# Optimization experiments

Measured on AMD Instinct MI355X. Metric: run time of the kernel, lower is better.

Reference implementation:

```python
import jax, jax.numpy as jnp
import numpy as np

B, T, E, NH = 2, 2048, 512, 8
HD = E // NH
SCALE = float(HD) ** -0.5


def setup_inputs() -> dict:
    key = jax.random.key(0)
    ks = jax.random.split(key, 7)
    s = 0.02
    return {
        "x": jax.random.normal(ks[0], (B, T, E), dtype=jnp.float32),
        "w_qkv": jax.random.normal(ks[1], (E, 3 * E), dtype=jnp.float32) * s,
        "b_qkv": jax.random.normal(ks[2], (3 * E,), dtype=jnp.float32) * s,
        "w_od": jax.random.normal(ks[3], (E, 2 * NH), dtype=jnp.float32) * s,
        "b_od": jax.random.normal(ks[4], (2 * NH,), dtype=jnp.float32) * s,
        "w_out": jax.random.normal(ks[5], (E, E), dtype=jnp.float32) * s,
        "b_out": jax.random.normal(ks[6], (E,), dtype=jnp.float32) * s,
    }


def _heads(t):  # (B,T,E) -> (B*NH, T, HD)
    return t.reshape(B, T, NH, HD).transpose(0, 2, 1, 3).reshape(B * NH, T, HD)


def _point_mask(idx, j):  # idx: (B*NH,T) float indices -> one-hot (B*NH,T,T)
    return (j[None, None, :] == idx[:, :, None]).astype(jnp.float32)


def reference(x, w_qkv, b_qkv, w_od, b_od, w_out, b_out):
    qkv = x @ w_qkv + b_qkv
    Q, K, V = jnp.split(qkv, 3, axis=-1)  # each (B,T,E)

    od = Q @ w_od + b_od  # (B,T,2*NH)
    offset, duration = jnp.split(od, 2, axis=-1)
    offset = jnp.tanh(offset) * T
    duration = jax.nn.sigmoid(duration) * T

    query_index = jnp.arange(T, dtype=x.dtype)[None, :, None]  # (1,T,1)
    anchor = query_index + offset  # (B,T,NH)
    # 'b t nh -> (b nh) t'
    anchor = anchor.transpose(0, 2, 1).reshape(B * NH, T)
    duration = duration.transpose(0, 2, 1).reshape(B * NH, T)

    start = anchor - duration
    end = anchor + duration
    bound_l = jnp.floor(start)
    bound_r = jnp.ceil(end)
    anchor_l = jnp.floor(anchor)
    anchor_r = anchor_l + 1.0

    j = jnp.arange(T, dtype=x.dtype)
    neg_bound_weight = (bound_l - start)[:, :, None] * _point_mask(bound_l, j) \
                     + (end - bound_r)[:, :, None] * _point_mask(bound_r, j)
    anchor_dist_l = anchor - anchor_l
    anchor_weight = anchor_dist_l[:, :, None] * _point_mask(anchor_r, j) \
                  + (1.0 - anchor_dist_l)[:, :, None] * _point_mask(anchor_l, j)
    point_weight = 1.0 + neg_bound_weight + anchor_weight  # (B*NH,T,T)

    # segment mask: True OUTSIDE [bound_l, bound_r]
    attn_mask = (j[None, None, :] < bound_l[:, :, None]) | (j[None, None, :] > bound_r[:, :, None])

    Qh, Kh, Vh = _heads(Q), _heads(K), _heads(V)  # (B*NH, T, HD)
    scores = jnp.einsum('bic,brc->bir', Qh, Kh) * SCALE * point_weight
    scores = jnp.where(attn_mask, jnp.asarray(-1e8, scores.dtype), scores)
    attn = jax.nn.softmax(scores, axis=-1)
    out = jnp.einsum('bir,brc->bic', attn, Vh)  # (B*NH,T,HD)
    out = out.reshape(B, NH, T, HD).transpose(0, 2, 1, 3).reshape(B, T, E)
    return out @ w_out + b_out
```

## Files before the change

### kernel.cpp

```cpp
#include <hip/hip_runtime.h>
#include <math.h>

typedef float vf4 __attribute__((ext_vector_type(4)));
typedef float f32x4 __attribute__((ext_vector_type(4)));
typedef short bf16x8 __attribute__((ext_vector_type(8)));
typedef short short4v __attribute__((ext_vector_type(4)));
typedef int int2v __attribute__((ext_vector_type(2)));
typedef int int4v __attribute__((ext_vector_type(4)));

constexpr int B = 2, T = 2048, E = 512, NH = 8, HD = 64;
constexpr int BH = B * NH;
constexpr int NT = BH * T;
constexpr int KSPLIT = 4;
constexpr float SCALE = 0.125f;
constexpr float LOG2E = 1.44269504088896f;
constexpr float QSC = SCALE * LOG2E;

static __device__ __forceinline__ short f2bf(float f) {
  unsigned u = __float_as_uint(f);
  unsigned r = (u + 0x7fffu + ((u >> 16) & 1u)) >> 16;
  return (short)r;
}
static __device__ __forceinline__ unsigned pk2bf(float a, float b) {
  unsigned lo = (unsigned)(unsigned short)f2bf(a);
  unsigned hi = (unsigned)(unsigned short)f2bf(b);
  return lo | (hi << 16);
}
static __device__ __forceinline__ unsigned pkhu(float a, float b) {
  unsigned ua = __float_as_uint(a) + 0x8000u;
  unsigned ub = __float_as_uint(b) + 0x8000u;
  return __builtin_amdgcn_perm(ub, ua, 0x07060302u);
}
#if __has_builtin(__builtin_amdgcn_exp2f)
#define EXP2F(x) __builtin_amdgcn_exp2f(x)
#else
#define EXP2F(x) exp2f(x)
#endif
static __device__ __forceinline__ float bf2f(short s) {
  return __uint_as_float(((unsigned)(unsigned short)s) << 16);
}

__global__ __launch_bounds__(256) void prep_all(
    const float* __restrict__ x, const float* __restrict__ w_qkv,
    const float* __restrict__ b_qkv, const float* __restrict__ w_od,
    const float* __restrict__ b_od,
    short* __restrict__ xb, short* __restrict__ wTq, short* __restrict__ wTo,
    const float* __restrict__ w_out, float* __restrict__ Wc,
    float* __restrict__ bc)
{
  __shared__ float sh[8464];
  const int bid = blockIdx.x;
  const int tid = threadIdx.x;

  if (bid < 2048) {
    int idx = (bid * 256 + tid) * 4;
    vf4 v = *(const vf4*)&x[idx];
    short4v o;
    o[0] = f2bf(v[0]); o[1] = f2bf(v[1]); o[2] = f2bf(v[2]); o[3] = f2bf(v[3]);
    *(short4v*)&xb[idx] = o;
  } else if (bid < 3072) {
    const float* w; short* wT; int N, t;
    if (bid < 2816) { t = bid - 2048; w = w_qkv; wT = wTq; N = 1536; }
    else            { t = bid - 2816; w = w_out; wT = wTo; N = 512; }
    float (*tt)[33] = (float(*)[33])sh;
    const int k0 = (t & 15) * 32;
    const int n0 = (t >> 4) * 32;
    const int c = tid & 31, r = tid >> 5;
#pragma unroll
    for (int p = 0; p < 4; ++p)
      tt[r + p * 8][c] = w[(size_t)(k0 + r + p * 8) * N + n0 + c];
    __syncthreads();
#pragma unroll
    for (int p = 0; p < 4; ++p)
      wT[(size_t)(n0 + r + p * 8) * 512 + k0 + c] = f2bf(tt[c][r + p * 8]);
  } else {
    float* Lod = sh;
    float (*pb)[17] = (float(*)[17])(sh + 8192);
    const int bx = bid - 3072;
#pragma unroll
    for (int p = 0; p < 8; ++p) {
      int idx = (p * 256 + tid) * 4;
      *(vf4*)&Lod[idx] = *(const vf4*)&w_od[idx];
    }
    __syncthreads();
    if (bx < 32) {
      const int k = bx * 16 + (tid >> 4);
      const int c = tid & 15;
      float s = 0.0f;
      for (int m = 0; m < E; m += 4) {
        vf4 wq = *(const vf4*)&w_qkv[(size_t)k * 1536 + m];
        s += wq[0] * Lod[(m + 0) * 16 + c] + wq[1] * Lod[(m + 1) * 16 + c]
           + wq[2] * Lod[(m + 2) * 16 + c] + wq[3] * Lod[(m + 3) * 16 + c];
      }
      Wc[k * 16 + c] = s;
    } else {
      const int c = tid & 15, seg = tid >> 4;
      float s = 0.0f;
      for (int m = seg * 32; m < seg * 32 + 32; ++m)
        s += b_qkv[m] * Lod[m * 16 + c];
      pb[seg][c] = s;
      __syncthreads();
      if (tid < 16) {
        float acc = b_od[tid];
#pragma unroll
        for (int g = 0; g < 16; ++g) acc += pb[g][tid];
        bc[tid] = acc;
      }
    }
  }
}

__global__ __launch_bounds__(256) void qkv_od(
    const short* __restrict__ xb, const short* __restrict__ wT,
    const float* __restrict__ bias, short* __restrict__ qkvb,
    short* __restrict__ Vtg,
    const float* __restrict__ x, const float* __restrict__ Wc,
    const float* __restrict__ bc, float* __restrict__ prm)
{
  __shared__ __align__(16) short smem_s[16896];
  const int bid = blockIdx.x;
  const int tid = threadIdx.x;

  if (bid < 768) {
    const int wave = tid >> 6, lane = tid & 63;
    const int quad = lane >> 4, l15 = lane & 15;
    const int wm = wave >> 1, wn = wave & 1;
    const int bx = bid % 24, by = bid / 24;
    const int m0 = by * 128, n0 = bx * 64;

    f32x4 acc[4][2];
#pragma unroll
    for (int mi = 0; mi < 4; ++mi)
#pragma unroll
      for (int ni = 0; ni < 2; ++ni) acc[mi][ni] = (f32x4){0, 0, 0, 0};

    const int sr = tid >> 1, sc = (tid & 1) * 16;
    const int br2 = tid >> 2, bk2 = (tid & 3) * 8;

#define QLD(R, K0) do {                                                   \
      R[0] = *(const bf16x8*)&xb[(size_t)(m0 + sr) * 512 + (K0) + sc];    \
      R[1] = *(const bf16x8*)&xb[(size_t)(m0 + sr) * 512 + (K0) + sc + 8];\
      R[2] = *(const bf16x8*)&wT[(size_t)(n0 + br2) * 512 + (K0) + bk2];  \
    } while (0)
#define QST(BUF, R) do {                                                  \
      short* As_ = smem_s + (BUF) * 7680;                                 \
      short* Bt_ = As_ + 5120;                                            \
      *(bf16x8*)&As_[sr * 40 + sc] = R[0];                                \
      *(bf16x8*)&As_[sr * 40 + sc + 8] = R[1];                            \
      *(bf16x8*)&Bt_[br2 * 40 + bk2] = R[2];                              \
    } while (0)
#define QMM(BUF) do {                                                     \
      const short* As_ = smem_s + (BUF) * 7680;                           \
      const short* Bt_ = As_ + 5120;                                      \
      bf16x8 aA[4], bB[2];                                                \
      for (int mi = 0; mi < 4; ++mi)                                      \
        aA[mi] = *(const bf16x8*)&As_[(wm * 64 + mi * 16 + l15) * 40 + quad * 8]; \
      for (int ni = 0; ni < 2; ++ni)                                      \
        bB[ni] = *(const bf16x8*)&Bt_[(wn * 32 + ni * 16 + l15) * 40 + quad * 8]; \
      for (int mi = 0; mi < 4; ++mi)                                      \
        for (int ni = 0; ni < 2; ++ni)                                    \
          acc[mi][ni] = __builtin_amdgcn_mfma_f32_16x16x32_bf16(          \
              aA[mi], bB[ni], acc[mi][ni], 0, 0, 0);                      \
    } while (0)

    bf16x8 rA[3], rB[3];
    QLD(rA, 0); QST(0, rA);
    QLD(rA, 32);
    __syncthreads();
#pragma unroll 1
    for (int k0 = 0; k0 < 512; k0 += 64) {
      if (k0 + 64 < 512) QLD(rB, k0 + 64);
      QMM(0);
      QST(1, rA);
      __syncthreads();
      if (k0 + 96 < 512) QLD(rA, k0 + 96);
      QMM(1);
      if (k0 + 64 < 512) { QST(0, rB); __syncthreads(); }
    }
#undef QLD
#undef QST
#undef QMM

#pragma unroll
    for (int mi = 0; mi < 4; ++mi)
#pragma unroll
      for (int ni = 0; ni < 2; ++ni) {
        const int col = n0 + wn * 32 + ni * 16 + l15;
        const int rowb = m0 + wm * 64 + mi * 16 + quad * 4;
        const float bs = bias[col];
        if (col < 1024) {
          const float qs = (col < 512) ? QSC : 1.0f;
#pragma unroll
          for (int r = 0; r < 4; ++r)
            qkvb[(size_t)(rowb + r) * 1536 + col] =
                f2bf((acc[mi][ni][r] + bs) * qs);
        } else {
          const int h = (col - 1024) >> 6, hd = col & 63;
          const int b = rowb >> 11, tt = rowb & 2047;
          int2v pk;
          pk[0] = (int)pk2bf(acc[mi][ni][0] + bs, acc[mi][ni][1] + bs);
          pk[1] = (int)pk2bf(acc[mi][ni][2] + bs, acc[mi][ni][3] + bs);
          *(int2v*)&Vtg[(size_t)(((b << 3) + h) * 64 + hd) * T + tt] = pk;
        }
      }
  } else {
    float* Lod = (float*)smem_s;
    float* ods = ((float*)smem_s) + 8192;
    const int obx = bid - 768;
#pragma unroll
    for (int p = 0; p < 8; ++p) {
      int idx = (p * 256 + tid) * 4;
      *(vf4*)&Lod[idx] = *(const vf4*)&Wc[idx];
    }
    __syncthreads();

    const int r = tid >> 4, c = tid & 15;
    const int row = obx * 16 + r;
    float sum = bc[c];
    const float* qr = x + (size_t)row * E;
    for (int k = 0; k < E; k += 4) {
      vf4 q = *(const vf4*)&qr[k];
      sum += q[0] * Lod[(k + 0) * 16 + c]
           + q[1] * Lod[(k + 1) * 16 + c]
           + q[2] * Lod[(k + 2) * 16 + c]
           + q[3] * Lod[(k + 3) * 16 + c];
    }
    ods[r * 16 + c] = sum;
    __syncthreads();

    if (tid < 128) {
      const int rr = tid >> 3, h = tid & 7;
      const int grow = obx * 16 + rr;
      const int b = grow / T, i = grow % T;
      float o = ods[rr * 16 + h];
      float d = ods[rr * 16 + h + 8];
      float offset   = tanhf(o) * (float)T;
      float duration = (float)T / (1.0f + expf(-d));
      float anchor = (float)i + offset;
      float start = anchor - duration;
      float end   = anchor + duration;
      float bl = floorf(start);
      float br = ceilf(end);
      float al = floorf(anchor);
      float wbl = bl - start;
      float wbr = end - br;
      float af  = anchor - al;
      float rsc = 1.0f;
      if (br < 0.0f || bl > (float)(T - 1)) {
        bl = 0.0f; br = (float)(T - 1);
        wbl = 0.0f; wbr = 0.0f; al = -5.0f; af = 0.0f;
        rsc = 0.0f;
      }
      int idx = (b * NH + h) * T + i;
      prm[0 * NT + idx] = bl;
      prm[1 * NT + idx] = br;
      prm[2 * NT + idx] = wbl;
      prm[3 * NT + idx] = wbr;
      prm[4 * NT + idx] = al;
      prm[5 * NT + idx] = af;
      prm[6 * NT + idx] = rsc;
    }
  }
}

__global__ __launch_bounds__(256, 4) void flash_attn_mfma6(
    const short* __restrict__ qkvb, const short* __restrict__ Vtg,
    const float* __restrict__ prm,
    short* __restrict__ Opart, float* __restrict__ lpart)
{
  __shared__ __align__(16) short Ks[2][64 * 72];
  __shared__ __align__(16) short Vt[2][64 * 72];
  __shared__ __align__(16) short Ps[4][16 * 72];
  __shared__ float u_s[8];

  const int tid = threadIdx.x;
  const int wave = tid >> 6, lane = tid & 63;
  const int quad = lane >> 4, l15 = lane & 15;
  const int qt = blockIdx.x, bh = blockIdx.y, ks = blockIdx.z;
  const int b = bh >> 3, h = bh & 7;
  const int i0 = qt * 64;
  const int i = i0 + wave * 16 + l15;

  const int pidx = bh * T + i;
  float blf = prm[0 * NT + pidx];
  float brf = prm[1 * NT + pidx];
  float wbl = prm[2 * NT + pidx];
  float wbr = prm[3 * NT + pidx];
  float alf = prm[4 * NT + pidx];
  float afr = prm[5 * NT + pidx];
  float rsc = prm[6 * NT + pidx];
  const int bli = (int)blf, widi = (int)brf - bli, ali = (int)alf;
  const unsigned widu = (unsigned)widi;
  const float a1 = 1.0f - afr;

  bf16x8 aQ0, aQ1;
  {
    size_t bq = (size_t)(b * T + i) * 1536 + h * 64;
    aQ0 = *(const bf16x8*)&qkvb[bq + quad * 8];
    aQ1 = *(const bf16x8*)&qkvb[bq + 32 + quad * 8];
    if (rsc == 0.0f) {
      bf16x8 z = {0, 0, 0, 0, 0, 0, 0, 0};
      aQ0 = z; aQ1 = z;
    }
  }

  float bmn = blf, bmx = brf;
#pragma unroll
  for (int d = 1; d < 64; d <<= 1) {
    bmn = fminf(bmn, __shfl_xor(bmn, d));
    bmx = fmaxf(bmx, __shfl_xor(bmx, d));
  }
  if (lane == 0) { u_s[wave * 2] = bmn; u_s[wave * 2 + 1] = bmx; }
  __syncthreads();
  bmn = fminf(fminf(u_s[0], u_s[2]), fminf(u_s[4], u_s[6]));
  bmx = fmaxf(fmaxf(u_s[1], u_s[3]), fmaxf(u_s[5], u_s[7]));
  const int ktlo = max(ks * 8, max(((int)bmn) >> 6, 0));
  const int kthi = min(ks * 8 + 7, min(((int)bmx) >> 6, T / 64 - 1));

  f32x4 o[4];
#pragma unroll
  for (int c = 0; c < 4; ++c) o[c] = (f32x4){0, 0, 0, 0};
  f32x4 lq = (f32x4){0, 0, 0, 0};
  const short BF1 = (short)0x3F80;
  const bf16x8 vone = {BF1, BF1, BF1, BF1, BF1, BF1, BF1, BF1};

  const int rq = tid >> 3, cb = (tid & 7) * 8;
  const short* kbase = qkvb + (size_t)b * T * 1536 + 512 + h * 64 + cb;
  const short* vbase = Vtg + (size_t)bh * 64 * T + cb;

#define FLD(R, KT) do { int j_ = (KT) * 64;                              \
    R[0] = *(const bf16x8*)&kbase[(size_t)(j_ + rq) * 1536];             \
    R[1] = *(const bf16x8*)&kbase[(size_t)(j_ + 32 + rq) * 1536];        \
    R[2] = *(const bf16x8*)&vbase[(size_t)rq * T + j_];                  \
    R[3] = *(const bf16x8*)&vbase[(size_t)(32 + rq) * T + j_];           \
  } while (0)
#define FST(BUF, R) do {                                                 \
    *(bf16x8*)&Ks[BUF][rq * 72 + cb] = R[0];                             \
    *(bf16x8*)&Ks[BUF][(32 + rq) * 72 + cb] = R[1];                      \
    *(bf16x8*)&Vt[BUF][rq * 72 + cb] = R[2];                             \
    *(bf16x8*)&Vt[BUF][(32 + rq) * 72 + cb] = R[3];                      \
  } while (0)

  auto compute = [&](int bufc, int ktc) {
    const int j0 = ktc * 64;
    const short* KsB = Ks[bufc];
    const short* VtB = Vt[bufc];

    f32x4 s[4];
#pragma unroll
    for (int nc = 0; nc < 4; ++nc) {
      const short* kb = &KsB[(nc * 16 + l15) * 72 + quad * 8];
      f32x4 a = (f32x4){0, 0, 0, 0};
      a = __builtin_amdgcn_mfma_f32_16x16x32_bf16(*(const bf16x8*)&kb[0],  aQ0, a, 0, 0, 0);
      a = __builtin_amdgcn_mfma_f32_16x16x32_bf16(*(const bf16x8*)&kb[32], aQ1, a, 0, 0, 0);
      s[nc] = a;
    }

    const int clean = (bli < j0) & (bli + widi > j0 + 63) &
                      ((ali > j0 + 63) | (ali + 1 < j0));
    if (__all(clean)) {
#pragma unroll
      for (int nc = 0; nc < 4; ++nc) {
        float p0 = EXP2F(s[nc][0]);
        float p1 = EXP2F(s[nc][1]);
        float p2 = EXP2F(s[nc][2]);
        float p3 = EXP2F(s[nc][3]);
        int2v pk;
        pk[0] = (int)pkhu(p0, p1);
        pk[1] = (int)pkhu(p2, p3);
        *(int2v*)&Ps[wave][l15 * 72 + nc * 16 + quad * 4] = pk;
      }
    } else {
      const int dq  = j0 + quad * 4 - bli;
      const int dq2 = j0 + quad * 4 - ali;
#pragma unroll
      for (int nc = 0; nc < 4; ++nc) {
        const int dn = dq + nc * 16, d2n = dq2 + nc * 16;
        float pr[4];
#pragma unroll
        for (int r = 0; r < 4; ++r) {
          int d = dn + r, d2 = d2n + r;
          float e  = (d == 0) ? wbl : ((d == widi) ? wbr : 0.0f);
          float aw = (d2 == 0) ? a1 : ((d2 == 1) ? afr : 0.0f);
          float w = 1.0f + e + aw;
          float v = s[nc][r] * w;
          v = ((unsigned)d <= widu) ? v : -115.0f;
          pr[r] = EXP2F(v);
        }
        int2v pk;
        pk[0] = (int)pkhu(pr[0], pr[1]);
        pk[1] = (int)pkhu(pr[2], pr[3]);
        *(int2v*)&Ps[wave][l15 * 72 + nc * 16 + quad * 4] = pk;
      }
    }

    bf16x8 bP0 = *(const bf16x8*)&Ps[wave][l15 * 72 + quad * 8];
    bf16x8 bP1 = *(const bf16x8*)&Ps[wave][l15 * 72 + 32 + quad * 8];
    lq = __builtin_amdgcn_mfma_f32_16x16x32_bf16(vone, bP0, lq, 0, 0, 0);
    lq = __builtin_amdgcn_mfma_f32_16x16x32_bf16(vone, bP1, lq, 0, 0, 0);
#pragma unroll
    for (int nc2 = 0; nc2 < 4; ++nc2) {
      const short* vb = &VtB[(nc2 * 16 + l15) * 72 + quad * 8];
      o[nc2] = __builtin_amdgcn_mfma_f32_16x16x32_bf16(
          *(const bf16x8*)&vb[0],  bP0, o[nc2], 0, 0, 0);
      o[nc2] = __builtin_amdgcn_mfma_f32_16x16x32_bf16(
          *(const bf16x8*)&vb[32], bP1, o[nc2], 0, 0, 0);
    }
  };

  if (ktlo <= kthi) {
    bf16x8 rA[4], rB[4];
    FLD(rA, ktlo);
    FST(0, rA);
    if (ktlo + 1 <= kthi) FLD(rA, ktlo + 1);
    __syncthreads();
    int buf = 0, kt = ktlo;
    while (true) {
      if (kt + 2 <= kthi) FLD(rB, kt + 2);
      compute(buf, kt);
      if (kt == kthi) break;
      FST(buf ^ 1, rA);
      __syncthreads();
      buf ^= 1; ++kt;
      if (kt + 2 <= kthi) FLD(rA, kt + 2);
      compute(buf, kt);
      if (kt == kthi) break;
      FST(buf ^ 1, rB);
      __syncthreads();
      buf ^= 1; ++kt;
    }
  }
#undef FLD
#undef FST

  if (lane < 16)
    lpart[ks * NT + bh * T + i] = lq[0];

  size_t ob = (size_t)ks * (B * T * E) + (size_t)(b * T + i) * E + h * 64;
#pragma unroll
  for (int nc2 = 0; nc2 < 4; ++nc2) {
    int2v pk;
    pk[0] = (int)pk2bf(o[nc2][0], o[nc2][1]);
    pk[1] = (int)pk2bf(o[nc2][2], o[nc2][3]);
    *(int2v*)&Opart[ob + nc2 * 16 + quad * 4] = pk;
  }
}

__global__ __launch_bounds__(256) void combine_attn(
    const short* __restrict__ Opart, const float* __restrict__ lpart,
    short* __restrict__ attnb)
{
  int base = (blockIdx.x * 256 + threadIdx.x) * 8;
  int row = base >> 9;
  int c = base & 511;
  int h = c >> 6;
  int b = row >> 11;
  int i = row & (T - 1);
  int lidx = ((b << 3) + h) * T + i;
  float l = (lpart[lidx] + lpart[NT + lidx]) +
            (lpart[2 * NT + lidx] + lpart[3 * NT + lidx]);
  float inv = 1.0f / l;
  bf16x8 o0 = *(const bf16x8*)&Opart[base];
  bf16x8 o1 = *(const bf16x8*)&Opart[(size_t)(B * T * E) + base];
  bf16x8 o2 = *(const bf16x8*)&Opart[(size_t)(2 * B * T * E) + base];
  bf16x8 o3 = *(const bf16x8*)&Opart[(size_t)(3 * B * T * E) + base];
  int4v ov;
#pragma unroll
  for (int j = 0; j < 4; ++j) {
    float a = ((bf2f(o0[2 * j]) + bf2f(o1[2 * j])) +
               (bf2f(o2[2 * j]) + bf2f(o3[2 * j]))) * inv;
    float bb = ((bf2f(o0[2 * j + 1]) + bf2f(o1[2 * j + 1])) +
                (bf2f(o2[2 * j + 1]) + bf2f(o3[2 * j + 1]))) * inv;
    ov[j] = (int)pk2bf(a, bb);
  }
  *(int4v*)&attnb[base] = ov;
}

__global__ __launch_bounds__(256) void out_gemm_bf16(
    const short* __restrict__ Ab, const short* __restrict__ wT,
    const float* __restrict__ bias, float* __restrict__ Co)
{
  __shared__ __align__(16) short smem_o[10240];

  const int tid = threadIdx.x;
  const int wave = tid >> 6, lane = tid & 63;
  const int quad = lane >> 4, l15 = lane & 15;
  const int wm = wave >> 1, wn = wave & 1;
  const int m0 = blockIdx.y * 64, n0 = blockIdx.x * 64;

  f32x4 acc[2][2];
#pragma unroll
  for (int mi = 0; mi < 2; ++mi)
#pragma unroll
    for (int ni = 0; ni < 2; ++ni) acc[mi][ni] = (f32x4){0, 0, 0, 0};

  const int ar = tid >> 2, akc = (tid & 3) * 8;

#define OLD(R, K0) do {                                                  \
    R[0] = *(const bf16x8*)&Ab[(size_t)(m0 + ar) * 512 + (K0) + akc];    \
    R[1] = *(const bf16x8*)&wT[(size_t)(n0 + ar) * 512 + (K0) + akc];    \
  } while (0)
#define OST(BUF, R) do {                                                 \
    short* As_ = smem_o + (BUF) * 5120;                                  \
    short* Bt_ = As_ + 2560;                                             \
    *(bf16x8*)&As_[ar * 40 + akc] = R[0];                                \
    *(bf16x8*)&Bt_[ar * 40 + akc] = R[1];                                \
  } while (0)
#define OMM(BUF) do {                                                    \
    const short* As_ = smem_o + (BUF) * 5120;                            \
    const short* Bt_ = As_ + 2560;                                       \
    bf16x8 aA[2], bB[2];                                                 \
    for (int mi = 0; mi < 2; ++mi)                                       \
      aA[mi] = *(const bf16x8*)&As_[(wm * 32 + mi * 16 + l15) * 40 + quad * 8]; \
    for (int ni = 0; ni < 2; ++ni)                                       \
      bB[ni] = *(const bf16x8*)&Bt_[(wn * 32 + ni * 16 + l15) * 40 + quad * 8]; \
    for (int mi = 0; mi < 2; ++mi)                                       \
      for (int ni = 0; ni < 2; ++ni)                                     \
        acc[mi][ni] = __builtin_amdgcn_mfma_f32_16x16x32_bf16(           \
            aA[mi], bB[ni], acc[mi][ni], 0, 0, 0);                       \
  } while (0)

  bf16x8 rA[2], rB[2];
  OLD(rA, 0); OST(0, rA);
  OLD(rA, 32);
  __syncthreads();
#pragma unroll 1
  for (int k0 = 0; k0 < 512; k0 += 64) {
    if (k0 + 64 < 512) OLD(rB, k0 + 64);
    OMM(0);
    OST(1, rA);
    __syncthreads();
    if (k0 + 96 < 512) OLD(rA, k0 + 96);
    OMM(1);
    if (k0 + 64 < 512) { OST(0, rB); __syncthreads(); }
  }
#undef OLD
#undef OST
#undef OMM

#pragma unroll
  for (int mi = 0; mi < 2; ++mi)
#pragma unroll
    for (int ni = 0; ni < 2; ++ni)
#pragma unroll
      for (int r = 0; r < 4; ++r) {
        int row = m0 + wm * 32 + mi * 16 + quad * 4 + r;
        int col = n0 + wn * 32 + ni * 16 + l15;
        Co[(size_t)row * 512 + col] = acc[mi][ni][r] + bias[col];
      }
}

extern "C" void kernel_launch(void* const* d_in, const int* in_sizes, int n_in,
                              void* d_out, int out_size, void* d_ws, size_t ws_size,
                              hipStream_t stream)
{
  const float* x     = (const float*)d_in[0];
  const float* w_qkv = (const float*)d_in[1];
  const float* b_qkv = (const float*)d_in[2];
  const float* w_od  = (const float*)d_in[3];
  const float* b_od  = (const float*)d_in[4];
  const float* w_out = (const float*)d_in[5];
  const float* b_out = (const float*)d_in[6];
  float* out = (float*)d_out;

  char* w = (char*)d_ws;
  short* xb    = (short*)w;  w += (size_t)B * T * E * 2;
  short* wTq   = (short*)w;  w += (size_t)E * 3 * E * 2;
  short* wTo   = (short*)w;  w += (size_t)E * E * 2;
  short* qkvb  = (short*)w;  w += (size_t)B * T * 3 * E * 2;
  short* Vtg   = (short*)w;  w += (size_t)B * T * E * 2;
  float* Wc    = (float*)w;  w += (size_t)E * 16 * 4;
  float* bc    = (float*)w;  w += 256;
  float* prm   = (float*)w;  w += (size_t)7 * NT * 4;
  short* Opart = (short*)w;  w += (size_t)KSPLIT * B * T * E * 2;
  float* lpart = (float*)w;  w += (size_t)KSPLIT * NT * 4;
  short* attnb = (short*)w;  w += (size_t)B * T * E * 2;

  prep_all<<<dim3(3105), 256, 0, stream>>>(
      x, w_qkv, b_qkv, w_od, b_od, xb, wTq, wTo, w_out, Wc, bc);

  qkv_od<<<dim3(1024), 256, 0, stream>>>(
      xb, wTq, b_qkv, qkvb, Vtg, x, Wc, bc, prm);

  flash_attn_mfma6<<<dim3(T / 64, BH, KSPLIT), 256, 0, stream>>>(
      qkvb, Vtg, prm, Opart, lpart);

  combine_attn<<<dim3(B * T * E / 2048), 256, 0, stream>>>(Opart, lpart, attnb);

  out_gemm_bf16<<<dim3(E / 64, B * T / 64), 256, 0, stream>>>(
      attnb, wTo, b_out, out);
}
```

Baseline: 203.0 us.

## Fuse split-K combine into output GEMM and simplify attention prefetch loop

The separate combine_attn kernel is removed. Its work (summing four partial O slabs and dividing by the row normaliser) now happens inside the output GEMM's A-tile load, which drops one kernel launch and the write/read round trip of the combined attention buffer. The flash-attention main loop is also rewritten from a two-stage register prefetch into a simpler one-tile-ahead loop with unroll 1. That shortens prefetch distance and may expose more global load latency. The fused GEMM now reads four Opart slabs per A tile across 8 column-tile blocks, so each partial is re-read 8 times, which could cost more bandwidth than the kernel it replaces.

```diff
diff --git a/kernel.cpp b/kernel.cpp
--- a/kernel.cpp
+++ b/kernel.cpp
@@ -263,7 +263,7 @@
   }
 }
 
-__global__ __launch_bounds__(256, 4) void flash_attn_mfma6(
+__global__ __launch_bounds__(256, 4) void flash_attn_mfma7(
     const short* __restrict__ qkvb, const short* __restrict__ Vtg,
     const float* __restrict__ prm,
     short* __restrict__ Opart, float* __restrict__ lpart)
@@ -328,23 +328,34 @@
   const short* kbase = qkvb + (size_t)b * T * 1536 + 512 + h * 64 + cb;
   const short* vbase = Vtg + (size_t)bh * 64 * T + cb;
 
-#define FLD(R, KT) do { int j_ = (KT) * 64;                              \
-    R[0] = *(const bf16x8*)&kbase[(size_t)(j_ + rq) * 1536];             \
-    R[1] = *(const bf16x8*)&kbase[(size_t)(j_ + 32 + rq) * 1536];        \
-    R[2] = *(const bf16x8*)&vbase[(size_t)rq * T + j_];                  \
-    R[3] = *(const bf16x8*)&vbase[(size_t)(32 + rq) * T + j_];           \
-  } while (0)
-#define FST(BUF, R) do {                                                 \
-    *(bf16x8*)&Ks[BUF][rq * 72 + cb] = R[0];                             \
-    *(bf16x8*)&Ks[BUF][(32 + rq) * 72 + cb] = R[1];                      \
-    *(bf16x8*)&Vt[BUF][rq * 72 + cb] = R[2];                             \
-    *(bf16x8*)&Vt[BUF][(32 + rq) * 72 + cb] = R[3];                      \
-  } while (0)
-
-  auto compute = [&](int bufc, int ktc) {
-    const int j0 = ktc * 64;
-    const short* KsB = Ks[bufc];
-    const short* VtB = Vt[bufc];
+  bf16x8 kr0, kr1, vr0, vr1;
+  if (ktlo <= kthi) {
+    const int j0 = ktlo * 64;
+    kr0 = *(const bf16x8*)&kbase[(size_t)(j0 + rq) * 1536];
+    kr1 = *(const bf16x8*)&kbase[(size_t)(j0 + 32 + rq) * 1536];
+    vr0 = *(const bf16x8*)&vbase[(size_t)rq * T + j0];
+    vr1 = *(const bf16x8*)&vbase[(size_t)(32 + rq) * T + j0];
+    *(bf16x8*)&Ks[0][rq * 72 + cb] = kr0;
+    *(bf16x8*)&Ks[0][(32 + rq) * 72 + cb] = kr1;
+    *(bf16x8*)&Vt[0][rq * 72 + cb] = vr0;
+    *(bf16x8*)&Vt[0][(32 + rq) * 72 + cb] = vr1;
+  }
+  __syncthreads();
+
+  int buf = 0;
+#pragma unroll 1
+  for (int kt = ktlo; kt <= kthi; ++kt) {
+    const int j0 = kt * 64;
+    if (kt < kthi) {
+      const int j1 = j0 + 64;
+      kr0 = *(const bf16x8*)&kbase[(size_t)(j1 + rq) * 1536];
+      kr1 = *(const bf16x8*)&kbase[(size_t)(j1 + 32 + rq) * 1536];
+      vr0 = *(const bf16x8*)&vbase[(size_t)rq * T + j1];
+      vr1 = *(const bf16x8*)&vbase[(size_t)(32 + rq) * T + j1];
+    }
+
+    const short* KsB = Ks[buf];
+    const short* VtB = Vt[buf];
 
     f32x4 s[4];
 #pragma unroll
@@ -406,32 +417,18 @@
       o[nc2] = __builtin_amdgcn_mfma_f32_16x16x32_bf16(
           *(const bf16x8*)&vb[32], bP1, o[nc2], 0, 0, 0);
     }
-  };
-
-  if (ktlo <= kthi) {
-    bf16x8 rA[4], rB[4];
-    FLD(rA, ktlo);
-    FST(0, rA);
-    if (ktlo + 1 <= kthi) FLD(rA, ktlo + 1);
-    __syncthreads();
-    int buf = 0, kt = ktlo;
-    while (true) {
-      if (kt + 2 <= kthi) FLD(rB, kt + 2);
-      compute(buf, kt);
-      if (kt == kthi) break;
-      FST(buf ^ 1, rA);
+
+    if (kt < kthi) {
+      short* Kn = Ks[buf ^ 1];
+      short* Vn = Vt[buf ^ 1];
+      *(bf16x8*)&Kn[rq * 72 + cb] = kr0;
+      *(bf16x8*)&Kn[(32 + rq) * 72 + cb] = kr1;
+      *(bf16x8*)&Vn[rq * 72 + cb] = vr0;
+      *(bf16x8*)&Vn[(32 + rq) * 72 + cb] = vr1;
       __syncthreads();
-      buf ^= 1; ++kt;
-      if (kt + 2 <= kthi) FLD(rA, kt + 2);
-      compute(buf, kt);
-      if (kt == kthi) break;
-      FST(buf ^ 1, rB);
-      __syncthreads();
-      buf ^= 1; ++kt;
-    }
-  }
-#undef FLD
-#undef FST
+      buf ^= 1;
+    }
+  }
 
   if (lane < 16)
     lpart[ks * NT + bh * T + i] = lq[0];
@@ -446,41 +443,13 @@
   }
 }
 
-__global__ __launch_bounds__(256) void combine_attn(
+__global__ __launch_bounds__(256) void out_gemm_fused(
     const short* __restrict__ Opart, const float* __restrict__ lpart,
-    short* __restrict__ attnb)
-{
-  int base = (blockIdx.x * 256 + threadIdx.x) * 8;
-  int row = base >> 9;
-  int c = base & 511;
-  int h = c >> 6;
-  int b = row >> 11;
-  int i = row & (T - 1);
-  int lidx = ((b << 3) + h) * T + i;
-  float l = (lpart[lidx] + lpart[NT + lidx]) +
-            (lpart[2 * NT + lidx] + lpart[3 * NT + lidx]);
-  float inv = 1.0f / l;
-  bf16x8 o0 = *(const bf16x8*)&Opart[base];
-  bf16x8 o1 = *(const bf16x8*)&Opart[(size_t)(B * T * E) + base];
-  bf16x8 o2 = *(const bf16x8*)&Opart[(size_t)(2 * B * T * E) + base];
-  bf16x8 o3 = *(const bf16x8*)&Opart[(size_t)(3 * B * T * E) + base];
-  int4v ov;
-#pragma unroll
-  for (int j = 0; j < 4; ++j) {
-    float a = ((bf2f(o0[2 * j]) + bf2f(o1[2 * j])) +
-               (bf2f(o2[2 * j]) + bf2f(o3[2 * j]))) * inv;
-    float bb = ((bf2f(o0[2 * j + 1]) + bf2f(o1[2 * j + 1])) +
-                (bf2f(o2[2 * j + 1]) + bf2f(o3[2 * j + 1]))) * inv;
-    ov[j] = (int)pk2bf(a, bb);
-  }
-  *(int4v*)&attnb[base] = ov;
-}
-
-__global__ __launch_bounds__(256) void out_gemm_bf16(
-    const short* __restrict__ Ab, const short* __restrict__ wT,
-    const float* __restrict__ bias, float* __restrict__ Co)
+    const short* __restrict__ wT, const float* __restrict__ bias,
+    float* __restrict__ Co)
 {
   __shared__ __align__(16) short smem_o[10240];
+  __shared__ float inv_s[64 * 8];
 
   const int tid = threadIdx.x;
   const int wave = tid >> 6, lane = tid & 63;
@@ -488,6 +457,19 @@
   const int wm = wave >> 1, wn = wave & 1;
   const int m0 = blockIdx.y * 64, n0 = blockIdx.x * 64;
 
+#pragma unroll
+  for (int p = 0; p < 2; ++p) {
+    int e = p * 256 + tid;
+    int row = e >> 3, hh = e & 7;
+    int grow = m0 + row;
+    int bb = grow >> 11, ii = grow & (T - 1);
+    int lidx = ((bb << 3) + hh) * T + ii;
+    float l = (lpart[lidx] + lpart[NT + lidx]) +
+              (lpart[2 * NT + lidx] + lpart[3 * NT + lidx]);
+    inv_s[e] = 1.0f / l;
+  }
+  __syncthreads();
+
   f32x4 acc[2][2];
 #pragma unroll
   for (int mi = 0; mi < 2; ++mi)
@@ -495,16 +477,32 @@
     for (int ni = 0; ni < 2; ++ni) acc[mi][ni] = (f32x4){0, 0, 0, 0};
 
   const int ar = tid >> 2, akc = (tid & 3) * 8;
+  constexpr size_t SLAB = (size_t)B * T * E;
 
 #define OLD(R, K0) do {                                                  \
-    R[0] = *(const bf16x8*)&Ab[(size_t)(m0 + ar) * 512 + (K0) + akc];    \
-    R[1] = *(const bf16x8*)&wT[(size_t)(n0 + ar) * 512 + (K0) + akc];    \
+    size_t abase = (size_t)(m0 + ar) * 512 + (K0) + akc;                 \
+    bf16x8 q0 = *(const bf16x8*)&Opart[abase];                           \
+    bf16x8 q1 = *(const bf16x8*)&Opart[SLAB + abase];                    \
+    bf16x8 q2 = *(const bf16x8*)&Opart[2 * SLAB + abase];                \
+    bf16x8 q3 = *(const bf16x8*)&Opart[3 * SLAB + abase];                \
+    float iv = inv_s[ar * 8 + (((K0) + akc) >> 6)];                      \
+    float fa[8];                                                         \
+    for (int j = 0; j < 8; ++j)                                          \
+      fa[j] = ((bf2f(q0[j]) + bf2f(q1[j])) +                             \
+               (bf2f(q2[j]) + bf2f(q3[j]))) * iv;                        \
+    int4v pk_;                                                           \
+    pk_[0] = (int)pk2bf(fa[0], fa[1]);                                   \
+    pk_[1] = (int)pk2bf(fa[2], fa[3]);                                   \
+    pk_[2] = (int)pk2bf(fa[4], fa[5]);                                   \
+    pk_[3] = (int)pk2bf(fa[6], fa[7]);                                   \
+    R0 = pk_;                                                            \
+    R1 = *(const bf16x8*)&wT[(size_t)(n0 + ar) * 512 + (K0) + akc];      \
   } while (0)
-#define OST(BUF, R) do {                                                 \
+#define OST(BUF) do {                                                    \
     short* As_ = smem_o + (BUF) * 5120;                                  \
     short* Bt_ = As_ + 2560;                                             \
-    *(bf16x8*)&As_[ar * 40 + akc] = R[0];                                \
-    *(bf16x8*)&Bt_[ar * 40 + akc] = R[1];                                \
+    *(int4v*)&As_[ar * 40 + akc] = R0;                                   \
+    *(bf16x8*)&Bt_[ar * 40 + akc] = R1;                                  \
   } while (0)
 #define OMM(BUF) do {                                                    \
     const short* As_ = smem_o + (BUF) * 5120;                            \
@@ -520,19 +518,22 @@
             aA[mi], bB[ni], acc[mi][ni], 0, 0, 0);                       \
   } while (0)
 
-  bf16x8 rA[2], rB[2];
-  OLD(rA, 0); OST(0, rA);
-  OLD(rA, 32);
+  int4v R0; bf16x8 R1;
+  OLD(, 0); OST(0);
+  OLD(, 32);
   __syncthreads();
 #pragma unroll 1
   for (int k0 = 0; k0 < 512; k0 += 64) {
-    if (k0 + 64 < 512) OLD(rB, k0 + 64);
     OMM(0);
-    OST(1, rA);
+    OST(1);
     __syncthreads();
-    if (k0 + 96 < 512) OLD(rA, k0 + 96);
+    if (k0 + 64 < 512) OLD(, k0 + 64);
     OMM(1);
-    if (k0 + 64 < 512) { OST(0, rB); __syncthreads(); }
+    if (k0 + 64 < 512) {
+      OST(0);
+      __syncthreads();
+      if (k0 + 96 < 512) OLD(, k0 + 96);
+    }
   }
 #undef OLD
 #undef OST
@@ -574,7 +575,6 @@
   float* prm   = (float*)w;  w += (size_t)7 * NT * 4;
   short* Opart = (short*)w;  w += (size_t)KSPLIT * B * T * E * 2;
   float* lpart = (float*)w;  w += (size_t)KSPLIT * NT * 4;
-  short* attnb = (short*)w;  w += (size_t)B * T * E * 2;
 
   prep_all<<<dim3(3105), 256, 0, stream>>>(
       x, w_qkv, b_qkv, w_od, b_od, xb, wTq, wTo, w_out, Wc, bc);
@@ -582,11 +582,9 @@
   qkv_od<<<dim3(1024), 256, 0, stream>>>(
       xb, wTq, b_qkv, qkvb, Vtg, x, Wc, bc, prm);
 
-  flash_attn_mfma6<<<dim3(T / 64, BH, KSPLIT), 256, 0, stream>>>(
+  flash_attn_mfma7<<<dim3(T / 64, BH, KSPLIT), 256, 0, stream>>>(
       qkvb, Vtg, prm, Opart, lpart);
 
-  combine_attn<<<dim3(B * T * E / 2048), 256, 0, stream>>>(Opart, lpart, attnb);
-
-  out_gemm_bf16<<<dim3(E / 64, B * T / 64), 256, 0, stream>>>(
-      attnb, wTo, b_out, out);
-}
+  out_gemm_fused<<<dim3(E / 64, B * T / 64), 256, 0, stream>>>(
+      Opart, lpart, wTo, b_out, out);
+}
```

Measured after the change: 181.0 us. 10.8% less time.

## Process two query row-blocks per wave to reuse K/V tiles in flash attention

Applied to the files above, without the earlier changes.

Each wave now handles 32 query rows (two 16-row groups) instead of 16, so every K and V fragment loaded from LDS feeds twice as many MFMAs, and the block covers 128 queries, halving the grid. The softmax row-sum is accumulated in registers with shuffles instead of an extra MFMA against a ones vector. The prefetch changes from a two-deep register pipeline to a single-step one, and launch bounds drop to 2 blocks per CU. The aim is to cut K/V load and LDS traffic per FLOP, at the cost of more registers, lower occupancy, fewer blocks, and a coarser K-range bound per block that may process more masked tiles.

```diff
diff --git a/kernel.cpp b/kernel.cpp
--- a/kernel.cpp
+++ b/kernel.cpp
@@ -263,14 +263,14 @@
   }
 }
 
-__global__ __launch_bounds__(256, 4) void flash_attn_mfma6(
+__global__ __launch_bounds__(256, 2) void flash_attn_mfma8(
     const short* __restrict__ qkvb, const short* __restrict__ Vtg,
     const float* __restrict__ prm,
     short* __restrict__ Opart, float* __restrict__ lpart)
 {
   __shared__ __align__(16) short Ks[2][64 * 72];
   __shared__ __align__(16) short Vt[2][64 * 72];
-  __shared__ __align__(16) short Ps[4][16 * 72];
+  __shared__ __align__(16) short Ps[4][32 * 72];
   __shared__ float u_s[8];
 
   const int tid = threadIdx.x;
@@ -278,33 +278,38 @@
   const int quad = lane >> 4, l15 = lane & 15;
   const int qt = blockIdx.x, bh = blockIdx.y, ks = blockIdx.z;
   const int b = bh >> 3, h = bh & 7;
-  const int i0 = qt * 64;
-  const int i = i0 + wave * 16 + l15;
-
-  const int pidx = bh * T + i;
-  float blf = prm[0 * NT + pidx];
-  float brf = prm[1 * NT + pidx];
-  float wbl = prm[2 * NT + pidx];
-  float wbr = prm[3 * NT + pidx];
-  float alf = prm[4 * NT + pidx];
-  float afr = prm[5 * NT + pidx];
-  float rsc = prm[6 * NT + pidx];
-  const int bli = (int)blf, widi = (int)brf - bli, ali = (int)alf;
-  const unsigned widu = (unsigned)widi;
-  const float a1 = 1.0f - afr;
-
-  bf16x8 aQ0, aQ1;
+  const int i0 = qt * 128;
+  const int ia = i0 + wave * 32 + l15;
+  const int ib = ia + 16;
+
+  const int pa = bh * T + ia, pb_ = pa + 16;
+  float blfA = prm[0 * NT + pa],  brfA = prm[1 * NT + pa];
+  float wblA = prm[2 * NT + pa],  wbrA = prm[3 * NT + pa];
+  float alfA = prm[4 * NT + pa],  afrA = prm[5 * NT + pa];
+  float rscA = prm[6 * NT + pa];
+  float blfB = prm[0 * NT + pb_], brfB = prm[1 * NT + pb_];
+  float wblB = prm[2 * NT + pb_], wbrB = prm[3 * NT + pb_];
+  float alfB = prm[4 * NT + pb_], afrB = prm[5 * NT + pb_];
+  float rscB = prm[6 * NT + pb_];
+  const int bliA = (int)blfA, widA = (int)brfA - bliA, aliA = (int)alfA;
+  const int bliB = (int)blfB, widB = (int)brfB - bliB, aliB = (int)alfB;
+  const unsigned widuA = (unsigned)widA, widuB = (unsigned)widB;
+  const float a1A = 1.0f - afrA, a1B = 1.0f - afrB;
+
+  bf16x8 aQ0a, aQ1a, aQ0b, aQ1b;
   {
-    size_t bq = (size_t)(b * T + i) * 1536 + h * 64;
-    aQ0 = *(const bf16x8*)&qkvb[bq + quad * 8];
-    aQ1 = *(const bf16x8*)&qkvb[bq + 32 + quad * 8];
-    if (rsc == 0.0f) {
-      bf16x8 z = {0, 0, 0, 0, 0, 0, 0, 0};
-      aQ0 = z; aQ1 = z;
-    }
-  }
-
-  float bmn = blf, bmx = brf;
+    size_t bqa = (size_t)(b * T + ia) * 1536 + h * 64;
+    aQ0a = *(const bf16x8*)&qkvb[bqa + quad * 8];
+    aQ1a = *(const bf16x8*)&qkvb[bqa + 32 + quad * 8];
+    size_t bqb = bqa + (size_t)16 * 1536;
+    aQ0b = *(const bf16x8*)&qkvb[bqb + quad * 8];
+    aQ1b = *(const bf16x8*)&qkvb[bqb + 32 + quad * 8];
+    bf16x8 z = {0, 0, 0, 0, 0, 0, 0, 0};
+    if (rscA == 0.0f) { aQ0a = z; aQ1a = z; }
+    if (rscB == 0.0f) { aQ0b = z; aQ1b = z; }
+  }
+
+  float bmn = fminf(blfA, blfB), bmx = fmaxf(brfA, brfB);
 #pragma unroll
   for (int d = 1; d < 64; d <<= 1) {
     bmn = fminf(bmn, __shfl_xor(bmn, d));
@@ -317,132 +322,170 @@
   const int ktlo = max(ks * 8, max(((int)bmn) >> 6, 0));
   const int kthi = min(ks * 8 + 7, min(((int)bmx) >> 6, T / 64 - 1));
 
-  f32x4 o[4];
-#pragma unroll
-  for (int c = 0; c < 4; ++c) o[c] = (f32x4){0, 0, 0, 0};
-  f32x4 lq = (f32x4){0, 0, 0, 0};
-  const short BF1 = (short)0x3F80;
-  const bf16x8 vone = {BF1, BF1, BF1, BF1, BF1, BF1, BF1, BF1};
+  f32x4 oA[4], oB[4];
+#pragma unroll
+  for (int c = 0; c < 4; ++c) { oA[c] = (f32x4){0, 0, 0, 0}; oB[c] = (f32x4){0, 0, 0, 0}; }
+  float laccA = 0.0f, laccB = 0.0f;
 
   const int rq = tid >> 3, cb = (tid & 7) * 8;
   const short* kbase = qkvb + (size_t)b * T * 1536 + 512 + h * 64 + cb;
   const short* vbase = Vtg + (size_t)bh * 64 * T + cb;
 
-#define FLD(R, KT) do { int j_ = (KT) * 64;                              \
-    R[0] = *(const bf16x8*)&kbase[(size_t)(j_ + rq) * 1536];             \
-    R[1] = *(const bf16x8*)&kbase[(size_t)(j_ + 32 + rq) * 1536];        \
-    R[2] = *(const bf16x8*)&vbase[(size_t)rq * T + j_];                  \
-    R[3] = *(const bf16x8*)&vbase[(size_t)(32 + rq) * T + j_];           \
-  } while (0)
-#define FST(BUF, R) do {                                                 \
-    *(bf16x8*)&Ks[BUF][rq * 72 + cb] = R[0];                             \
-    *(bf16x8*)&Ks[BUF][(32 + rq) * 72 + cb] = R[1];                      \
-    *(bf16x8*)&Vt[BUF][rq * 72 + cb] = R[2];                             \
-    *(bf16x8*)&Vt[BUF][(32 + rq) * 72 + cb] = R[3];                      \
-  } while (0)
-
-  auto compute = [&](int bufc, int ktc) {
-    const int j0 = ktc * 64;
-    const short* KsB = Ks[bufc];
-    const short* VtB = Vt[bufc];
-
-    f32x4 s[4];
+  bf16x8 kr0, kr1, vr0, vr1;
+  if (ktlo <= kthi) {
+    const int j0 = ktlo * 64;
+    kr0 = *(const bf16x8*)&kbase[(size_t)(j0 + rq) * 1536];
+    kr1 = *(const bf16x8*)&kbase[(size_t)(j0 + 32 + rq) * 1536];
+    vr0 = *(const bf16x8*)&vbase[(size_t)rq * T + j0];
+    vr1 = *(const bf16x8*)&vbase[(size_t)(32 + rq) * T + j0];
+    *(bf16x8*)&Ks[0][rq * 72 + cb] = kr0;
+    *(bf16x8*)&Ks[0][(32 + rq) * 72 + cb] = kr1;
+    *(bf16x8*)&Vt[0][rq * 72 + cb] = vr0;
+    *(bf16x8*)&Vt[0][(32 + rq) * 72 + cb] = vr1;
+  }
+  __syncthreads();
+
+  int buf = 0;
+#pragma unroll 1
+  for (int kt = ktlo; kt <= kthi; ++kt) {
+    const int j0 = kt * 64;
+    if (kt < kthi) {
+      const int j1 = j0 + 64;
+      kr0 = *(const bf16x8*)&kbase[(size_t)(j1 + rq) * 1536];
+      kr1 = *(const bf16x8*)&kbase[(size_t)(j1 + 32 + rq) * 1536];
+      vr0 = *(const bf16x8*)&vbase[(size_t)rq * T + j1];
+      vr1 = *(const bf16x8*)&vbase[(size_t)(32 + rq) * T + j1];
+    }
+
+    const short* KsB = Ks[buf];
+    const short* VtB = Vt[buf];
+
+    f32x4 sA[4], sB[4];
 #pragma unroll
     for (int nc = 0; nc < 4; ++nc) {
       const short* kb = &KsB[(nc * 16 + l15) * 72 + quad * 8];
+      bf16x8 k0 = *(const bf16x8*)&kb[0];
+      bf16x8 k1 = *(const bf16x8*)&kb[32];
       f32x4 a = (f32x4){0, 0, 0, 0};
-      a = __builtin_amdgcn_mfma_f32_16x16x32_bf16(*(const bf16x8*)&kb[0],  aQ0, a, 0, 0, 0);
-      a = __builtin_amdgcn_mfma_f32_16x16x32_bf16(*(const bf16x8*)&kb[32], aQ1, a, 0, 0, 0);
-      s[nc] = a;
-    }
-
-    const int clean = (bli < j0) & (bli + widi > j0 + 63) &
-                      ((ali > j0 + 63) | (ali + 1 < j0));
-    if (__all(clean)) {
+      a = __builtin_amdgcn_mfma_f32_16x16x32_bf16(k0, aQ0a, a, 0, 0, 0);
+      a = __builtin_amdgcn_mfma_f32_16x16x32_bf16(k1, aQ1a, a, 0, 0, 0);
+      sA[nc] = a;
+      f32x4 bq = (f32x4){0, 0, 0, 0};
+      bq = __builtin_amdgcn_mfma_f32_16x16x32_bf16(k0, aQ0b, bq, 0, 0, 0);
+      bq = __builtin_amdgcn_mfma_f32_16x16x32_bf16(k1, aQ1b, bq, 0, 0, 0);
+      sB[nc] = bq;
+    }
+
+    const int cleanA = (bliA < j0) & (bliA + widA > j0 + 63) &
+                       ((aliA > j0 + 63) | (aliA + 1 < j0));
+    const int cleanB = (bliB < j0) & (bliB + widB > j0 + 63) &
+                       ((aliB > j0 + 63) | (aliB + 1 < j0));
+    if (__all(cleanA & cleanB)) {
 #pragma unroll
       for (int nc = 0; nc < 4; ++nc) {
-        float p0 = EXP2F(s[nc][0]);
-        float p1 = EXP2F(s[nc][1]);
-        float p2 = EXP2F(s[nc][2]);
-        float p3 = EXP2F(s[nc][3]);
+        float p0 = EXP2F(sA[nc][0]);
+        float p1 = EXP2F(sA[nc][1]);
+        float p2 = EXP2F(sA[nc][2]);
+        float p3 = EXP2F(sA[nc][3]);
+        laccA += (p0 + p1) + (p2 + p3);
         int2v pk;
         pk[0] = (int)pkhu(p0, p1);
         pk[1] = (int)pkhu(p2, p3);
         *(int2v*)&Ps[wave][l15 * 72 + nc * 16 + quad * 4] = pk;
+        float q0 = EXP2F(sB[nc][0]);
+        float q1 = EXP2F(sB[nc][1]);
+        float q2 = EXP2F(sB[nc][2]);
+        float q3 = EXP2F(sB[nc][3]);
+        laccB += (q0 + q1) + (q2 + q3);
+        int2v pk2;
+        pk2[0] = (int)pkhu(q0, q1);
+        pk2[1] = (int)pkhu(q2, q3);
+        *(int2v*)&Ps[wave][(16 + l15) * 72 + nc * 16 + quad * 4] = pk2;
       }
     } else {
-      const int dq  = j0 + quad * 4 - bli;
-      const int dq2 = j0 + quad * 4 - ali;
+      const int base_j = j0 + quad * 4;
 #pragma unroll
       for (int nc = 0; nc < 4; ++nc) {
-        const int dn = dq + nc * 16, d2n = dq2 + nc * 16;
-        float pr[4];
+        const int jn = base_j + nc * 16;
+        float pr[4], qr2[4];
 #pragma unroll
         for (int r = 0; r < 4; ++r) {
-          int d = dn + r, d2 = d2n + r;
-          float e  = (d == 0) ? wbl : ((d == widi) ? wbr : 0.0f);
-          float aw = (d2 == 0) ? a1 : ((d2 == 1) ? afr : 0.0f);
-          float w = 1.0f + e + aw;
-          float v = s[nc][r] * w;
-          v = ((unsigned)d <= widu) ? v : -115.0f;
-          pr[r] = EXP2F(v);
+          int dA = jn + r - bliA, d2A = jn + r - aliA;
+          float eA  = (dA == 0) ? wblA : ((dA == widA) ? wbrA : 0.0f);
+          float awA = (d2A == 0) ? a1A : ((d2A == 1) ? afrA : 0.0f);
+          float vA = sA[nc][r] * (1.0f + eA + awA);
+          vA = ((unsigned)dA <= widuA) ? vA : -115.0f;
+          float pA = EXP2F(vA);
+          laccA += pA;
+          pr[r] = pA;
+          int dB = jn + r - bliB, d2B = jn + r - aliB;
+          float eB  = (dB == 0) ? wblB : ((dB == widB) ? wbrB : 0.0f);
+          float awB = (d2B == 0) ? a1B : ((d2B == 1) ? afrB : 0.0f);
+          float vB = sB[nc][r] * (1.0f + eB + awB);
+          vB = ((unsigned)dB <= widuB) ? vB : -115.0f;
+          float pB = EXP2F(vB);
+          laccB += pB;
+          qr2[r] = pB;
         }
         int2v pk;
         pk[0] = (int)pkhu(pr[0], pr[1]);
         pk[1] = (int)pkhu(pr[2], pr[3]);
         *(int2v*)&Ps[wave][l15 * 72 + nc * 16 + quad * 4] = pk;
+        int2v pk2;
+        pk2[0] = (int)pkhu(qr2[0], qr2[1]);
+        pk2[1] = (int)pkhu(qr2[2], qr2[3]);
+        *(int2v*)&Ps[wave][(16 + l15) * 72 + nc * 16 + quad * 4] = pk2;
       }
     }
 
-    bf16x8 bP0 = *(const bf16x8*)&Ps[wave][l15 * 72 + quad * 8];
-    bf16x8 bP1 = *(const bf16x8*)&Ps[wave][l15 * 72 + 32 + quad * 8];
-    lq = __builtin_amdgcn_mfma_f32_16x16x32_bf16(vone, bP0, lq, 0, 0, 0);
-    lq = __builtin_amdgcn_mfma_f32_16x16x32_bf16(vone, bP1, lq, 0, 0, 0);
+    bf16x8 bP0a = *(const bf16x8*)&Ps[wave][l15 * 72 + quad * 8];
+    bf16x8 bP1a = *(const bf16x8*)&Ps[wave][l15 * 72 + 32 + quad * 8];
+    bf16x8 bP0b = *(const bf16x8*)&Ps[wave][(16 + l15) * 72 + quad * 8];
+    bf16x8 bP1b = *(const bf16x8*)&Ps[wave][(16 + l15) * 72 + 32 + quad * 8];
 #pragma unroll
     for (int nc2 = 0; nc2 < 4; ++nc2) {
       const short* vb = &VtB[(nc2 * 16 + l15) * 72 + quad * 8];
-      o[nc2] = __builtin_amdgcn_mfma_f32_16x16x32_bf16(
-          *(const bf16x8*)&vb[0],  bP0, o[nc2], 0, 0, 0);
-      o[nc2] = __builtin_amdgcn_mfma_f32_16x16x32_bf16(
-          *(const bf16x8*)&vb[32], bP1, o[nc2], 0, 0, 0);
-    }
-  };
-
-  if (ktlo <= kthi) {
-    bf16x8 rA[4], rB[4];
-    FLD(rA, ktlo);
-    FST(0, rA);
-    if (ktlo + 1 <= kthi) FLD(rA, ktlo + 1);
-    __syncthreads();
-    int buf = 0, kt = ktlo;
-    while (true) {
-      if (kt + 2 <= kthi) FLD(rB, kt + 2);
-      compute(buf, kt);
-      if (kt == kthi) break;
-      FST(buf ^ 1, rA);
+      bf16x8 v0 = *(const bf16x8*)&vb[0];
+      bf16x8 v1 = *(const bf16x8*)&vb[32];
+      oA[nc2] = __builtin_amdgcn_mfma_f32_16x16x32_bf16(v0, bP0a, oA[nc2], 0, 0, 0);
+      oA[nc2] = __builtin_amdgcn_mfma_f32_16x16x32_bf16(v1, bP1a, oA[nc2], 0, 0, 0);
+      oB[nc2] = __builtin_amdgcn_mfma_f32_16x16x32_bf16(v0, bP0b, oB[nc2], 0, 0, 0);
+      oB[nc2] = __builtin_amdgcn_mfma_f32_16x16x32_bf16(v1, bP1b, oB[nc2], 0, 0, 0);
+    }
+
+    if (kt < kthi) {
+      short* Kn = Ks[buf ^ 1];
+      short* Vn = Vt[buf ^ 1];
+      *(bf16x8*)&Kn[rq * 72 + cb] = kr0;
+      *(bf16x8*)&Kn[(32 + rq) * 72 + cb] = kr1;
+      *(bf16x8*)&Vn[rq * 72 + cb] = vr0;
+      *(bf16x8*)&Vn[(32 + rq) * 72 + cb] = vr1;
       __syncthreads();
-      buf ^= 1; ++kt;
-      if (kt + 2 <= kthi) FLD(rA, kt + 2);
-      compute(buf, kt);
-      if (kt == kthi) break;
-      FST(buf ^ 1, rB);
-      __syncthreads();
-      buf ^= 1; ++kt;
-    }
-  }
-#undef FLD
-#undef FST
-
-  if (lane < 16)
-    lpart[ks * NT + bh * T + i] = lq[0];
-
-  size_t ob = (size_t)ks * (B * T * E) + (size_t)(b * T + i) * E + h * 64;
+      buf ^= 1;
+    }
+  }
+
+  laccA += __shfl_xor(laccA, 16);
+  laccA += __shfl_xor(laccA, 32);
+  laccB += __shfl_xor(laccB, 16);
+  laccB += __shfl_xor(laccB, 32);
+  if (lane < 16) {
+    lpart[ks * NT + bh * T + ia] = laccA;
+    lpart[ks * NT + bh * T + ib] = laccB;
+  }
+
+  size_t obA = (size_t)ks * (B * T * E) + (size_t)(b * T + ia) * E + h * 64;
+  size_t obB = (size_t)ks * (B * T * E) + (size_t)(b * T + ib) * E + h * 64;
 #pragma unroll
   for (int nc2 = 0; nc2 < 4; ++nc2) {
     int2v pk;
-    pk[0] = (int)pk2bf(o[nc2][0], o[nc2][1]);
-    pk[1] = (int)pk2bf(o[nc2][2], o[nc2][3]);
-    *(int2v*)&Opart[ob + nc2 * 16 + quad * 4] = pk;
+    pk[0] = (int)pk2bf(oA[nc2][0], oA[nc2][1]);
+    pk[1] = (int)pk2bf(oA[nc2][2], oA[nc2][3]);
+    *(int2v*)&Opart[obA + nc2 * 16 + quad * 4] = pk;
+    int2v pk2;
+    pk2[0] = (int)pk2bf(oB[nc2][0], oB[nc2][1]);
+    pk2[1] = (int)pk2bf(oB[nc2][2], oB[nc2][3]);
+    *(int2v*)&Opart[obB + nc2 * 16 + quad * 4] = pk2;
   }
 }
 
@@ -582,7 +625,7 @@
   qkv_od<<<dim3(1024), 256, 0, stream>>>(
       xb, wTq, b_qkv, qkvb, Vtg, x, Wc, bc, prm);
 
-  flash_attn_mfma6<<<dim3(T / 64, BH, KSPLIT), 256, 0, stream>>>(
+  flash_attn_mfma8<<<dim3(T / 128, BH, KSPLIT), 256, 0, stream>>>(
       qkvb, Vtg, prm, Opart, lpart);
 
   combine_attn<<<dim3(B * T * E / 2048), 256, 0, stream>>>(Opart, lpart, attnb);
```

New measurement: 165.2 us. -18.6%, faster.
